# Kernel tuning notes

Hardware: AMD Instinct MI355X
Metric: run time of the kernel (lower is better)

## Reference

```python
import jax, jax.numpy as jnp
import numpy as np


def setup_inputs() -> dict:
    key = jax.random.key(0)
    k1, k2 = jax.random.split(key)
    N, D, K = 131072, 256, 1024
    x = jax.random.normal(k1, (N, D), dtype=jnp.float32)
    centroids = jax.random.normal(k2, (K, D), dtype=jnp.float32)
    return {"x": x, "centroids": centroids}


def reference(x, centroids):
    """Nearest-centroid assignment with euclidean similarity (kmeans_pytorch euc_sim):
        sim[n,k] = 2 * x[n] . c[k] - |x[n]|^2 - |c[k]|^2  ( = -||x[n]-c[k]||^2 )
    Returns (max_sim [N], labels [N]).
    """
    # [N, K] similarity via single GEMM plus broadcast norms
    sim = (2.0 * jnp.einsum('nd,kd->nk', x, centroids)
           - jnp.sum(x * x, axis=-1, keepdims=True)
           - jnp.sum(centroids * centroids, axis=-1)[None, :])
    max_sim = jnp.max(sim, axis=-1)
    labels = jnp.argmax(sim, axis=-1)
    return max_sim, labels
```

## Files before the change

kernel.cpp:

```cpp
#include <hip/hip_runtime.h>

constexpr int N = 131072;
constexpr int D = 256;
constexpr int K = 1024;

constexpr int TM = 128;
constexpr int TK = 128;
constexpr float EPS = 0.08f;

typedef _Float16 f16x8 __attribute__((ext_vector_type(8)));
typedef float f32x4 __attribute__((ext_vector_type(4)));

__device__ _Float16 g_ctile[66 * 8192];

__device__ __forceinline__ float sqf(float a) { return __fmul_rn(a, a); }

__device__ __forceinline__ float np_sumsq128(const float* q) {
    float lane[16];
#pragma unroll
    for (int j = 0; j < 16; j++) {
        const float r0 = __fadd_rn(sqf(q[j]),      sqf(q[64 + j]));
        const float r1 = __fadd_rn(sqf(q[16 + j]), sqf(q[80 + j]));
        const float r2 = __fadd_rn(sqf(q[32 + j]), sqf(q[96 + j]));
        const float r3 = __fadd_rn(sqf(q[48 + j]), sqf(q[112 + j]));
        lane[j] = __fadd_rn(__fadd_rn(r0, r1), __fadd_rn(r2, r3));
    }
    float t[8];
#pragma unroll
    for (int i = 0; i < 8; i++) t[i] = __fadd_rn(lane[i], lane[i + 8]);
    float u[4];
#pragma unroll
    for (int i = 0; i < 4; i++) u[i] = __fadd_rn(t[i], t[i + 4]);
    return __fadd_rn(__fadd_rn(u[0], u[2]), __fadd_rn(u[1], u[3]));
}
__device__ __forceinline__ float np_pw256_sq(const float* p) {
    return __fadd_rn(np_sumsq128(p), np_sumsq128(p + 128));
}

__device__ __forceinline__ float np_dot256(const float* a, const float* b) {
    float A[4] = {0.f, 0.f, 0.f, 0.f};
#pragma unroll 4
    for (int t = 0; t < 16; t++) {
#pragma unroll
        for (int i = 3; i >= 0; i--) {
            const int base = 16 * t + 4 * i;
#pragma unroll
            for (int j = 0; j < 4; j++)
                A[j] = __fadd_rn(A[j], __fmul_rn(a[base + j], b[base + j]));
        }
    }
    return __fadd_rn(__fadd_rn(A[0], A[1]), __fadd_rn(A[2], A[3]));
}

#define SPL(vec, comp, he, le, idx)                                  \
    {                                                                \
        const float fv_ = (vec).comp;                                \
        const _Float16 hh_ = (_Float16)fv_;                          \
        he[idx] = hh_;                                               \
        le[idx] = (_Float16)(fv_ - (float)hh_);                      \
    }

__global__ __launch_bounds__(256) void prep_kernel(const float* __restrict__ c,
                                                   float* __restrict__ cn) {
    const int idx = blockIdx.x * 256 + threadIdx.x;
    const int kglob = idx >> 5;
    const int dslot = idx & 31;
    const int dc = dslot >> 2, kg = dslot & 3;
    const float* src = c + (size_t)kglob * D + dc * 32 + kg * 8;
    const float4 s0 = ((const float4*)src)[0];
    const float4 s1 = ((const float4*)src)[1];
    f16x8 h, l;
    SPL(s0, x, h, l, 0) SPL(s0, y, h, l, 1) SPL(s0, z, h, l, 2) SPL(s0, w, h, l, 3)
    SPL(s1, x, h, l, 4) SPL(s1, y, h, l, 5) SPL(s1, z, h, l, 6) SPL(s1, w, h, l, 7)
    const int kblk = kglob >> 7, krow = kglob & 127;
    const int st = kblk * 8 + dc;
    _Float16* base = g_ctile + (size_t)st * 8192;
    *(f16x8*)&base[kg * 1024 + krow * 8]        = h;
    *(f16x8*)&base[4096 + kg * 1024 + krow * 8] = l;
    if (idx < K) cn[idx] = np_pw256_sq(c + (size_t)idx * D);
}

#define WAITVM(n) asm volatile("s_waitcnt vmcnt(" #n ")" ::: "memory")

__global__ __launch_bounds__(256, 2) void fast_kernel(const float* __restrict__ x,
                                                      const float* __restrict__ c,
                                                      const float* __restrict__ cn,
                                                      float* __restrict__ out,
                                                      int* __restrict__ cnt,
                                                      int* __restrict__ list) {
    __shared__ _Float16 cs[4][8192] __attribute__((aligned(16)));
    __shared__ float cn_sh[K];
    __shared__ float xn_sh[TM];
    __shared__ int   rbi[TM];
    __shared__ int   rok[TM];

    const int t    = threadIdx.x;
    const int n0   = blockIdx.x * TM;
    const int lane = t & 63;
    const int w    = t >> 6;
    const int wrow = w * 32;
    const int lr   = lane & 15;
    const int lg   = lane >> 4;

#define STAGE(buf_, sidx_)                                                          \
    {                                                                               \
        const _Float16* gp_ = g_ctile + (size_t)(sidx_) * 8192 + t * 8;             \
        _Float16* lp_ = &cs[buf_][t * 8];                                           \
        _Pragma("unroll")                                                           \
        for (int u_ = 0; u_ < 4; u_++)                                              \
            __builtin_amdgcn_global_load_lds(                                       \
                (const __attribute__((address_space(1))) void*)(gp_ + u_ * 2048),   \
                (__attribute__((address_space(3))) void*)(lp_ + u_ * 2048),         \
                16, 0, 0);                                                          \
    }

    STAGE(0, 0);
    STAGE(1, 1);

#pragma unroll
    for (int q = 0; q < 4; q++) cn_sh[t + 256 * q] = cn[t + 256 * q];
    if (t < TM) xn_sh[t] = np_pw256_sq(x + (size_t)(n0 + t) * D);

    f16x8 ah[2][8], al[2][8];
#pragma unroll
    for (int st = 0; st < 8; st++)
#pragma unroll
        for (int i = 0; i < 2; i++) {
            const float* src = x + (size_t)(n0 + wrow + 16 * i + lr) * D + st * 32 + lg * 8;
            const float4 s0 = ((const float4*)src)[0];
            const float4 s1 = ((const float4*)src)[1];
            f16x8 h, l;
            SPL(s0, x, h, l, 0) SPL(s0, y, h, l, 1) SPL(s0, z, h, l, 2) SPL(s0, w, h, l, 3)
            SPL(s1, x, h, l, 4) SPL(s1, y, h, l, 5) SPL(s1, z, h, l, 6) SPL(s1, w, h, l, 7)
            ah[i][st] = h; al[i][st] = l;
        }

    float v1[8], v2[8];
    int   i1[8];
#pragma unroll
    for (int s = 0; s < 8; s++) {
        v1[s] = -__builtin_inff(); v2[s] = -__builtin_inff(); i1[s] = 0;
    }

    __syncthreads();

    for (int kb = 0; kb < 8; kb++) {
        f32x4 acc[2][8];
#pragma unroll
        for (int i = 0; i < 2; i++)
#pragma unroll
            for (int j = 0; j < 8; j++) acc[i][j] = (f32x4)(0.f);

#pragma unroll
        for (int dc8 = 0; dc8 < 8; dc8++) {
            const int s = kb * 8 + dc8;
            STAGE((dc8 + 2) & 3, s + 2);
            WAITVM(8);
            __builtin_amdgcn_s_barrier();
            __builtin_amdgcn_sched_barrier(0);
            asm volatile("" ::: "memory");

            const _Float16* csb = &cs[dc8 & 3][0];
            __builtin_amdgcn_s_setprio(1);
#pragma unroll
            for (int j = 0; j < 8; j++) {
                const f16x8 bh = *(const f16x8*)&csb[lg * 1024 + (16 * j + lr) * 8];
                const f16x8 bl = *(const f16x8*)&csb[4096 + lg * 1024 + (16 * j + lr) * 8];
                acc[0][j] = __builtin_amdgcn_mfma_f32_16x16x32_f16(ah[0][dc8], bh, acc[0][j], 0, 0, 0);
                acc[1][j] = __builtin_amdgcn_mfma_f32_16x16x32_f16(ah[1][dc8], bh, acc[1][j], 0, 0, 0);
                acc[0][j] = __builtin_amdgcn_mfma_f32_16x16x32_f16(al[0][dc8], bh, acc[0][j], 0, 0, 0);
                acc[1][j] = __builtin_amdgcn_mfma_f32_16x16x32_f16(al[1][dc8], bh, acc[1][j], 0, 0, 0);
                acc[0][j] = __builtin_amdgcn_mfma_f32_16x16x32_f16(ah[0][dc8], bl, acc[0][j], 0, 0, 0);
                acc[1][j] = __builtin_amdgcn_mfma_f32_16x16x32_f16(ah[1][dc8], bl, acc[1][j], 0, 0, 0);
            }
            __builtin_amdgcn_s_setprio(0);
            asm volatile("" ::: "memory");
        }

#pragma unroll
        for (int j = 0; j < 8; j++) {
            const int kg_ = kb * TK + 16 * j + lr;
            const float cnj = cn_sh[kg_];
#pragma unroll
            for (int i = 0; i < 2; i++)
#pragma unroll
                for (int r = 0; r < 4; r++) {
                    const int s = 4 * i + r;
                    const float v = 2.0f * acc[i][j][r] - xn_sh[wrow + 16 * i + 4 * lg + r] - cnj;
                    if (v > v1[s])       { v2[s] = v1[s]; v1[s] = v; i1[s] = kg_; }
                    else if (v > v2[s])  { v2[s] = v; }
                    else if (v == v1[s]) { v2[s] = v; }
                }
        }
    }

#pragma unroll
    for (int i = 0; i < 2; i++)
#pragma unroll
        for (int r = 0; r < 4; r++) {
            const int s = 4 * i + r;
            float a1v = v1[s], a2v = v2[s];
            int   ai  = i1[s];
#pragma unroll
            for (int m = 1; m <= 8; m <<= 1) {
                const float ov1 = __shfl_xor(a1v, m);
                const int   oi  = __shfl_xor(ai, m);
                const float ov2 = __shfl_xor(a2v, m);
                if (ov1 > a1v)      { a2v = fmaxf(a1v, ov2); a1v = ov1; ai = oi; }
                else if (ov1 < a1v) { a2v = fmaxf(a2v, ov1); }
                else                { ai = min(ai, oi); a2v = a1v; }
            }
            if (lr == 0) {
                const int row = wrow + 16 * i + 4 * lg + r;
                const int ok = (a1v - a2v >= EPS) ? 1 : 0;
                rbi[row] = ai;
                rok[row] = ok;
                if (!ok) { const int pos = atomicAdd(cnt, 1); list[pos] = n0 + row; }
            }
        }
    __syncthreads();

    if (t < TM && rok[t]) {
        const int row = n0 + t;
        const int bi  = rbi[t];
        const float dot = np_dot256(x + (size_t)row * D, c + (size_t)bi * D);
        const float v = __fsub_rn(__fsub_rn(__fmul_rn(2.0f, dot), xn_sh[t]), cn[bi]);
        out[row]     = v;
        out[N + row] = (float)bi;
    }
}

__global__ __launch_bounds__(256) void fallback_kernel(const float* __restrict__ x,
                                                       const float* __restrict__ c,
                                                       const float* __restrict__ cn,
                                                       float* __restrict__ out,
                                                       const int* __restrict__ cnt,
                                                       const int* __restrict__ list) {
    __shared__ float xrow[D];
    __shared__ float xn_s;
    __shared__ float wv[4];
    __shared__ int   wi[4];
    const int tid = threadIdx.x, lane = tid & 63, w = tid >> 6;
    const int total = *cnt;
    for (int idx = blockIdx.x; idx < total; idx += gridDim.x) {
        const int row = list[idx];
        if (tid < 64) *(float4*)&xrow[4 * tid] = ((const float4*)(x + (size_t)row * D))[tid];
        __syncthreads();
        if (tid == 0) xn_s = np_pw256_sq(xrow);
        __syncthreads();
        const float xn = xn_s;
        float bv = -__builtin_inff();
        int   bi = 0;
#pragma unroll
        for (int j = 0; j < 4; j++) {
            const int k = 4 * tid + j;
            const float dot = np_dot256(xrow, c + (size_t)k * D);
            const float v = __fsub_rn(__fsub_rn(__fmul_rn(2.0f, dot), xn), cn[k]);
            if (v > bv) { bv = v; bi = k; }
        }
#pragma unroll
        for (int m = 1; m <= 32; m <<= 1) {
            const float ov = __shfl_xor(bv, m);
            const int   oi = __shfl_xor(bi, m);
            if (ov > bv || (ov == bv && oi < bi)) { bv = ov; bi = oi; }
        }
        if (lane == 0) { wv[w] = bv; wi[w] = bi; }
        __syncthreads();
        if (tid == 0) {
#pragma unroll
            for (int ww = 1; ww < 4; ww++) {
                if (wv[ww] > bv || (wv[ww] == bv && wi[ww] < bi)) { bv = wv[ww]; bi = wi[ww]; }
            }
            out[row]     = bv;
            out[N + row] = (float)bi;
        }
        __syncthreads();
    }
}

extern "C" void kernel_launch(void* const* d_in, const int* in_sizes, int n_in,
                              void* d_out, int out_size, void* d_ws, size_t ws_size,
                              hipStream_t stream) {
    const float* x = (const float*)d_in[0];
    const float* c = (const float*)d_in[1];
    float* out     = (float*)d_out;
    float* cn = (float*)d_ws;
    int* cnt  = (int*)((char*)d_ws + 4096);
    int* list = (int*)((char*)d_ws + 4608);

    hipMemsetAsync(cnt, 0, sizeof(int), stream);
    prep_kernel<<<128, 256, 0, stream>>>(c, cn);
    fast_kernel<<<N / TM, 256, 0, stream>>>(x, c, cn, out, cnt, list);
    fallback_kernel<<<1024, 256, 0, stream>>>(x, c, cn, out, cnt, list);
}
```

Before: 566.0 us.

## Pre-split x into fp16 hi/lo tiles and stream through LDS with smaller K tiles

The prep kernel now also converts every x row into fp16 hi/lo halves laid out in MFMA-ready tiles in a global scratch buffer. The main kernel then bulk-loads its whole 128-row x tile into LDS with direct global-to-LDS loads instead of holding split fragments in registers. The centroid tile shrinks to 64 columns with double buffering, and the launch-bounds occupancy hint is dropped. This is meant to cut register pressure and the in-kernel split work. In exchange it adds a full extra write and read of a fp16 copy of x (about 128 MB) plus more barriers per step, and the large LDS footprint limits occupancy.

```diff
diff --git a/kernel.cpp b/kernel.cpp
--- a/kernel.cpp
+++ b/kernel.cpp
@@ -5,13 +5,14 @@
 constexpr int K = 1024;
 
 constexpr int TM = 128;
-constexpr int TK = 128;
+constexpr int TK = 64;
 constexpr float EPS = 0.08f;
 
 typedef _Float16 f16x8 __attribute__((ext_vector_type(8)));
 typedef float f32x4 __attribute__((ext_vector_type(4)));
 
-__device__ _Float16 g_ctile[66 * 8192];
+__device__ _Float16 g_ctile[130 * 4096];
+__device__ _Float16 g_xtile[(size_t)1024 * 65536];
 
 __device__ __forceinline__ float sqf(float a) { return __fmul_rn(a, a); }
 
@@ -60,35 +61,53 @@
         le[idx] = (_Float16)(fv_ - (float)hh_);                      \
     }
 
-__global__ __launch_bounds__(256) void prep_kernel(const float* __restrict__ c,
+__global__ __launch_bounds__(256) void prep_kernel(const float* __restrict__ x,
+                                                   const float* __restrict__ c,
                                                    float* __restrict__ cn) {
-    const int idx = blockIdx.x * 256 + threadIdx.x;
-    const int kglob = idx >> 5;
-    const int dslot = idx & 31;
-    const int dc = dslot >> 2, kg = dslot & 3;
-    const float* src = c + (size_t)kglob * D + dc * 32 + kg * 8;
-    const float4 s0 = ((const float4*)src)[0];
-    const float4 s1 = ((const float4*)src)[1];
-    f16x8 h, l;
-    SPL(s0, x, h, l, 0) SPL(s0, y, h, l, 1) SPL(s0, z, h, l, 2) SPL(s0, w, h, l, 3)
-    SPL(s1, x, h, l, 4) SPL(s1, y, h, l, 5) SPL(s1, z, h, l, 6) SPL(s1, w, h, l, 7)
-    const int kblk = kglob >> 7, krow = kglob & 127;
-    const int st = kblk * 8 + dc;
-    _Float16* base = g_ctile + (size_t)st * 8192;
-    *(f16x8*)&base[kg * 1024 + krow * 8]        = h;
-    *(f16x8*)&base[4096 + kg * 1024 + krow * 8] = l;
-    if (idx < K) cn[idx] = np_pw256_sq(c + (size_t)idx * D);
+    if (blockIdx.x < 16384) {
+        const int idx = blockIdx.x * 256 + threadIdx.x;
+        const int r = idx >> 5;
+        const int dslot = idx & 31;
+        const int ds = dslot >> 2, kg = dslot & 3;
+        const float* src = x + (size_t)r * D + ds * 32 + kg * 8;
+        const float4 s0 = ((const float4*)src)[0];
+        const float4 s1 = ((const float4*)src)[1];
+        f16x8 h, l;
+        SPL(s0, x, h, l, 0) SPL(s0, y, h, l, 1) SPL(s0, z, h, l, 2) SPL(s0, w, h, l, 3)
+        SPL(s1, x, h, l, 4) SPL(s1, y, h, l, 5) SPL(s1, z, h, l, 6) SPL(s1, w, h, l, 7)
+        const int blk = r >> 7, rrow = r & 127;
+        _Float16* base = g_xtile + (size_t)blk * 65536 + ds * 8192;
+        *(f16x8*)&base[rrow * 32 + kg * 8]        = h;
+        *(f16x8*)&base[4096 + rrow * 32 + kg * 8] = l;
+    } else {
+        const int idx = (blockIdx.x - 16384) * 256 + threadIdx.x;
+        const int kglob = idx >> 5;
+        const int dslot = idx & 31;
+        const int dc = dslot >> 2, kg = dslot & 3;
+        const float* src = c + (size_t)kglob * D + dc * 32 + kg * 8;
+        const float4 s0 = ((const float4*)src)[0];
+        const float4 s1 = ((const float4*)src)[1];
+        f16x8 h, l;
+        SPL(s0, x, h, l, 0) SPL(s0, y, h, l, 1) SPL(s0, z, h, l, 2) SPL(s0, w, h, l, 3)
+        SPL(s1, x, h, l, 4) SPL(s1, y, h, l, 5) SPL(s1, z, h, l, 6) SPL(s1, w, h, l, 7)
+        const int kb = kglob >> 6, col = kglob & 63;
+        _Float16* base = g_ctile + (size_t)(kb * 8 + dc) * 4096;
+        *(f16x8*)&base[col * 32 + kg * 8]        = h;
+        *(f16x8*)&base[2048 + col * 32 + kg * 8] = l;
+        if (idx < K) cn[idx] = np_pw256_sq(c + (size_t)idx * D);
+    }
 }
 
 #define WAITVM(n) asm volatile("s_waitcnt vmcnt(" #n ")" ::: "memory")
 
-__global__ __launch_bounds__(256, 2) void fast_kernel(const float* __restrict__ x,
-                                                      const float* __restrict__ c,
-                                                      const float* __restrict__ cn,
-                                                      float* __restrict__ out,
-                                                      int* __restrict__ cnt,
-                                                      int* __restrict__ list) {
-    __shared__ _Float16 cs[4][8192] __attribute__((aligned(16)));
+__global__ __launch_bounds__(256) void fast_kernel(const float* __restrict__ x,
+                                                   const float* __restrict__ c,
+                                                   const float* __restrict__ cn,
+                                                   float* __restrict__ out,
+                                                   int* __restrict__ cnt,
+                                                   int* __restrict__ list) {
+    __shared__ _Float16 as_[8 * 8192] __attribute__((aligned(16)));
+    __shared__ _Float16 cs[2][4096] __attribute__((aligned(16)));
     __shared__ float cn_sh[K];
     __shared__ float xn_sh[TM];
     __shared__ int   rbi[TM];
@@ -102,18 +121,24 @@
     const int lr   = lane & 15;
     const int lg   = lane >> 4;
 
-#define STAGE(buf_, sidx_)                                                          \
+    const _Float16* gx = g_xtile + (size_t)blockIdx.x * 65536;
+#pragma unroll
+    for (int u = 0; u < 32; u++)
+        __builtin_amdgcn_global_load_lds(
+            (const __attribute__((address_space(1))) void*)(gx + u * 2048 + t * 8),
+            (__attribute__((address_space(3))) void*)(&as_[u * 2048 + t * 8]), 16, 0, 0);
+
+#define STAGE(buf_, s_)                                                             \
     {                                                                               \
-        const _Float16* gp_ = g_ctile + (size_t)(sidx_) * 8192 + t * 8;             \
+        const _Float16* gp_ = g_ctile + (size_t)(s_) * 4096 + t * 8;                \
         _Float16* lp_ = &cs[buf_][t * 8];                                           \
-        _Pragma("unroll")                                                           \
-        for (int u_ = 0; u_ < 4; u_++)                                              \
-            __builtin_amdgcn_global_load_lds(                                       \
-                (const __attribute__((address_space(1))) void*)(gp_ + u_ * 2048),   \
-                (__attribute__((address_space(3))) void*)(lp_ + u_ * 2048),         \
-                16, 0, 0);                                                          \
-    }
-
+        __builtin_amdgcn_global_load_lds(                                           \
+            (const __attribute__((address_space(1))) void*)gp_,                     \
+            (__attribute__((address_space(3))) void*)lp_, 16, 0, 0);                \
+        __builtin_amdgcn_global_load_lds(                                           \
+            (const __attribute__((address_space(1))) void*)(gp_ + 2048),            \
+            (__attribute__((address_space(3))) void*)(lp_ + 2048), 16, 0, 0);       \
+    }
     STAGE(0, 0);
     STAGE(1, 1);
 
@@ -121,20 +146,6 @@
     for (int q = 0; q < 4; q++) cn_sh[t + 256 * q] = cn[t + 256 * q];
     if (t < TM) xn_sh[t] = np_pw256_sq(x + (size_t)(n0 + t) * D);
 
-    f16x8 ah[2][8], al[2][8];
-#pragma unroll
-    for (int st = 0; st < 8; st++)
-#pragma unroll
-        for (int i = 0; i < 2; i++) {
-            const float* src = x + (size_t)(n0 + wrow + 16 * i + lr) * D + st * 32 + lg * 8;
-            const float4 s0 = ((const float4*)src)[0];
-            const float4 s1 = ((const float4*)src)[1];
-            f16x8 h, l;
-            SPL(s0, x, h, l, 0) SPL(s0, y, h, l, 1) SPL(s0, z, h, l, 2) SPL(s0, w, h, l, 3)
-            SPL(s1, x, h, l, 4) SPL(s1, y, h, l, 5) SPL(s1, z, h, l, 6) SPL(s1, w, h, l, 7)
-            ah[i][st] = h; al[i][st] = l;
-        }
-
     float v1[8], v2[8];
     int   i1[8];
 #pragma unroll
@@ -144,41 +155,48 @@
 
     __syncthreads();
 
-    for (int kb = 0; kb < 8; kb++) {
-        f32x4 acc[2][8];
+    for (int kb = 0; kb < 16; kb++) {
+        f32x4 acc[2][4];
 #pragma unroll
         for (int i = 0; i < 2; i++)
 #pragma unroll
-            for (int j = 0; j < 8; j++) acc[i][j] = (f32x4)(0.f);
-
-#pragma unroll
-        for (int dc8 = 0; dc8 < 8; dc8++) {
-            const int s = kb * 8 + dc8;
-            STAGE((dc8 + 2) & 3, s + 2);
-            WAITVM(8);
+            for (int j = 0; j < 4; j++) acc[i][j] = (f32x4)(0.f);
+
+#pragma unroll
+        for (int dc = 0; dc < 8; dc++) {
+            const int p = kb * 8 + dc;
+            WAITVM(2);
             __builtin_amdgcn_s_barrier();
             __builtin_amdgcn_sched_barrier(0);
             asm volatile("" ::: "memory");
 
-            const _Float16* csb = &cs[dc8 & 3][0];
+            const _Float16* asb = &as_[dc * 8192];
+            const _Float16* csb = &cs[dc & 1][0];
+            const f16x8 ah0 = *(const f16x8*)&asb[(wrow + lr) * 32 + lg * 8];
+            const f16x8 al0 = *(const f16x8*)&asb[4096 + (wrow + lr) * 32 + lg * 8];
+            const f16x8 ah1 = *(const f16x8*)&asb[(wrow + 16 + lr) * 32 + lg * 8];
+            const f16x8 al1 = *(const f16x8*)&asb[4096 + (wrow + 16 + lr) * 32 + lg * 8];
             __builtin_amdgcn_s_setprio(1);
 #pragma unroll
-            for (int j = 0; j < 8; j++) {
-                const f16x8 bh = *(const f16x8*)&csb[lg * 1024 + (16 * j + lr) * 8];
-                const f16x8 bl = *(const f16x8*)&csb[4096 + lg * 1024 + (16 * j + lr) * 8];
-                acc[0][j] = __builtin_amdgcn_mfma_f32_16x16x32_f16(ah[0][dc8], bh, acc[0][j], 0, 0, 0);
-                acc[1][j] = __builtin_amdgcn_mfma_f32_16x16x32_f16(ah[1][dc8], bh, acc[1][j], 0, 0, 0);
-                acc[0][j] = __builtin_amdgcn_mfma_f32_16x16x32_f16(al[0][dc8], bh, acc[0][j], 0, 0, 0);
-                acc[1][j] = __builtin_amdgcn_mfma_f32_16x16x32_f16(al[1][dc8], bh, acc[1][j], 0, 0, 0);
-                acc[0][j] = __builtin_amdgcn_mfma_f32_16x16x32_f16(ah[0][dc8], bl, acc[0][j], 0, 0, 0);
-                acc[1][j] = __builtin_amdgcn_mfma_f32_16x16x32_f16(ah[1][dc8], bl, acc[1][j], 0, 0, 0);
+            for (int j = 0; j < 4; j++) {
+                const f16x8 bh = *(const f16x8*)&csb[(16 * j + lr) * 32 + lg * 8];
+                const f16x8 bl = *(const f16x8*)&csb[2048 + (16 * j + lr) * 32 + lg * 8];
+                acc[0][j] = __builtin_amdgcn_mfma_f32_16x16x32_f16(ah0, bh, acc[0][j], 0, 0, 0);
+                acc[1][j] = __builtin_amdgcn_mfma_f32_16x16x32_f16(ah1, bh, acc[1][j], 0, 0, 0);
+                acc[0][j] = __builtin_amdgcn_mfma_f32_16x16x32_f16(al0, bh, acc[0][j], 0, 0, 0);
+                acc[1][j] = __builtin_amdgcn_mfma_f32_16x16x32_f16(al1, bh, acc[1][j], 0, 0, 0);
+                acc[0][j] = __builtin_amdgcn_mfma_f32_16x16x32_f16(ah0, bl, acc[0][j], 0, 0, 0);
+                acc[1][j] = __builtin_amdgcn_mfma_f32_16x16x32_f16(ah1, bl, acc[1][j], 0, 0, 0);
             }
             __builtin_amdgcn_s_setprio(0);
             asm volatile("" ::: "memory");
-        }
-
-#pragma unroll
-        for (int j = 0; j < 8; j++) {
+            __builtin_amdgcn_s_barrier();
+            asm volatile("" ::: "memory");
+            STAGE(dc & 1, p + 2);
+        }
+
+#pragma unroll
+        for (int j = 0; j < 4; j++) {
             const int kg_ = kb * TK + 16 * j + lr;
             const float cnj = cn_sh[kg_];
 #pragma unroll
@@ -289,7 +307,7 @@
     int* list = (int*)((char*)d_ws + 4608);
 
     hipMemsetAsync(cnt, 0, sizeof(int), stream);
-    prep_kernel<<<128, 256, 0, stream>>>(c, cn);
+    prep_kernel<<<16512, 256, 0, stream>>>(x, c, cn);
     fast_kernel<<<N / TM, 256, 0, stream>>>(x, c, cn, out, cnt, list);
     fallback_kernel<<<1024, 256, 0, stream>>>(x, c, cn, out, cnt, list);
 }
```

Measured after the change: 934.7 us. 1.65x slower.
